# Kernel tuning notes

Hardware: AMD Instinct MI355X
Metric: run time of the kernel (lower is better)

## Reference

```python
import jax, jax.numpy as jnp
import numpy as np

B, H, W, C = 2, 128, 128, 192
HEADS = 6
HD = C // HEADS
WS = 16
OWIN = int(WS * 0.5) + WS          # 24
PAD = (OWIN - WS) // 2             # 4
NQ = WS * WS
NK = OWIN * OWIN
EPS = 1e-6
HID = ((int(C * 2.667) + 7) // 8) * 8  # 512


def _rel_pos_index():
    cq = np.stack(np.meshgrid(np.arange(WS), np.arange(WS), indexing='ij')).reshape(2, -1)
    ck = np.stack(np.meshgrid(np.arange(OWIN), np.arange(OWIN), indexing='ij')).reshape(2, -1)
    rel = (ck[:, None, :] - cq[:, :, None]).transpose(1, 2, 0).astype(np.int64)  # (nq, nk, 2)
    rel[:, :, 0] += WS - 1
    rel[:, :, 1] += WS - 1
    rel[:, :, 0] *= WS + OWIN - 1
    return rel.sum(-1)  # (nq, nk)

RPI = jnp.asarray(_rel_pos_index())


def setup_inputs() -> dict:
    key = jax.random.key(0)
    ks = jax.random.split(key, 16)
    def w(k, shape, s=0.02):
        return jax.random.normal(k, shape, jnp.float32) * s
    return {
        'x': jax.random.normal(ks[0], (B, H * W, C), jnp.float32),
        'qkv_w': w(ks[1], (3 * C, C)), 'qkv_b': jnp.zeros((3 * C,), jnp.float32),
        'proj_w': w(ks[2], (C, C)), 'proj_b': jnp.zeros((C,), jnp.float32),
        'rpb': w(ks[3], ((WS + OWIN - 1) ** 2, HEADS)),
        'n1_w': jnp.ones((C,), jnp.float32), 'n1_b': jnp.zeros((C,), jnp.float32),
        'ls1': jnp.full((C,), 1e-6, jnp.float32),
        'n2_w': jnp.ones((C,), jnp.float32), 'n2_b': jnp.zeros((C,), jnp.float32),
        'ls2': jnp.full((C,), 1e-6, jnp.float32),
        'fcgv_w': w(ks[4], (2 * HID, C)), 'fcgv_b': jnp.zeros((2 * HID,), jnp.float32),
        'dw_w': w(ks[5], (HID, 1, 3, 3)), 'dw_b': jnp.zeros((HID,), jnp.float32),
        'dwd_w': w(ks[6], (HID, 1, 3, 3)), 'dwd_b': jnp.zeros((HID,), jnp.float32),
        'dil_scale': w(ks[7], (1,), 0.1),
        'fco_w': w(ks[8], (C, HID)), 'fco_b': jnp.zeros((C,), jnp.float32),
    }


def _iln(x, wgt, bias):
    # spatially-holistic LN: stats over (L, C); returns normed x and residual scale
    xf = x.astype(jnp.float32)
    mean = xf.mean(axis=(1, 2), keepdims=True)
    var = ((xf - mean) ** 2).mean(axis=(1, 2), keepdims=True)
    std = jnp.sqrt(var + EPS)
    scale = jnp.minimum(std, 2.0)  # std_ema buffer initialized to 1.0 (eval path)
    xn = (xf - mean) / scale
    return (xn * wgt + bias).astype(x.dtype), scale


def _oca(x, qkv_w, qkv_b, proj_w, proj_b, rpb):
    b = x.shape[0]
    nh, nw = H // WS, W // WS
    nwin = b * nh * nw
    qkv = x @ qkv_w.T + qkv_b
    q, k, v = jnp.split(qkv, 3, axis=-1)
    # non-overlapping query windows: (nwin, heads, nq, hd)
    qw = q.reshape(b, nh, WS, nw, WS, C).transpose(0, 1, 3, 2, 4, 5)
    qw = qw.reshape(nwin, NQ, HEADS, HD).transpose(0, 2, 1, 3)
    # overlapping K/V windows via unfold(kernel=OWIN, stride=WS, pad=PAD)
    kv = jnp.concatenate([k, v], axis=-1).reshape(b, H, W, 2 * C).transpose(0, 3, 1, 2)
    kvp = jnp.pad(kv, ((0, 0), (0, 0), (PAD, PAD), (PAD, PAD)))
    ih = (jnp.arange(nh) * WS)[:, None] + jnp.arange(OWIN)[None, :]
    iw = (jnp.arange(nw) * WS)[:, None] + jnp.arange(OWIN)[None, :]
    kvw = kvp[:, :, ih][:, :, :, :, iw]               # (b, 2C, nh, owin, nw, owin)
    kvw = kvw.transpose(0, 2, 4, 3, 5, 1).reshape(nwin, NK, 2 * C)
    kw = kvw[..., :C].reshape(nwin, NK, HEADS, HD).transpose(0, 2, 1, 3)
    vw = kvw[..., C:].reshape(nwin, NK, HEADS, HD).transpose(0, 2, 1, 3)
    bias = rpb[RPI].transpose(2, 0, 1)                # (heads, nq, nk)
    logits = jnp.einsum('whqd,whkd->whqk', qw, kw) * (HD ** -0.5) + bias
    attn = jax.nn.softmax(logits, axis=-1)
    out = jnp.einsum('whqk,whkd->whqd', attn, vw)
    out = out.transpose(0, 2, 1, 3).reshape(nwin, NQ, C) @ proj_w.T + proj_b
    # window reverse -> (b, H*W, C)
    out = out.reshape(b, nh, nw, WS, WS, C).transpose(0, 1, 3, 2, 4, 5).reshape(b, H * W, C)
    return out


def _dw(x, wgt, bias, dil):
    y = jax.lax.conv_general_dilated(x, wgt, (1, 1), [(dil, dil), (dil, dil)],
                                     rhs_dilation=(dil, dil), feature_group_count=HID)
    return y + bias[None, :, None, None]


def _ffn(x, fcgv_w, fcgv_b, dw_w, dw_b, dwd_w, dwd_b, dil_scale, fco_w, fco_b):
    gv = x @ fcgv_w.T + fcgv_b
    g, val = jnp.split(gv, 2, axis=-1)
    h = jax.nn.silu(g) * val
    h = h.transpose(0, 2, 1).reshape(-1, HID, H, W)
    h = _dw(h, dw_w, dw_b, 1)
    h = h + dil_scale[0] * _dw(h, dwd_w, dwd_b, 2)
    h = h.reshape(-1, HID, H * W).transpose(0, 2, 1)
    return h @ fco_w.T + fco_b


def reference(x, qkv_w, qkv_b, proj_w, proj_b, rpb, n1_w, n1_b, ls1, n2_w, n2_b, ls2,
              fcgv_w, fcgv_b, dw_w, dw_b, dwd_w, dwd_b, dil_scale, fco_w, fco_b):
    xn, std1 = _iln(x, n1_w, n1_b)
    x = x + std1 * (ls1 * _oca(xn, qkv_w, qkv_b, proj_w, proj_b, rpb))
    xn2, std2 = _iln(x, n2_w, n2_b)
    x = x + std2 * (ls2 * _ffn(xn2, fcgv_w, fcgv_b, dw_w, dw_b, dwd_w, dwd_b, dil_scale, fco_w, fco_b))
    return x
```

## Files before the change

### kernel.cpp

```cpp
#include <hip/hip_runtime.h>

#define DI __device__ __forceinline__

typedef __attribute__((ext_vector_type(8))) short bh8;
typedef __attribute__((ext_vector_type(4))) float fx4;
typedef __attribute__((ext_vector_type(16))) float fx16;

DI short f2bf(float f) {
  unsigned u = __builtin_bit_cast(unsigned, f);
  u += 0x7FFFu + ((u >> 16) & 1u);
  return (short)(u >> 16);
}
DI float bf2f(short s) {
  unsigned u = ((unsigned)(unsigned short)s) << 16;
  return __builtin_bit_cast(float, u);
}
DI fx4 mfma16(bh8 a, bh8 b, fx4 c) {
  return __builtin_amdgcn_mfma_f32_16x16x32_bf16(a, b, c, 0, 0, 0);
}
DI fx16 mfma32(bh8 a, bh8 b, fx16 c) {
  return __builtin_amdgcn_mfma_f32_32x32x16_bf16(a, b, c, 0, 0, 0);
}
DI fx4 fzero() { fx4 z = {0.f, 0.f, 0.f, 0.f}; return z; }

DI float fexp2(float x) {
#if __has_builtin(__builtin_amdgcn_exp2f)
  return __builtin_amdgcn_exp2f(x);
#else
  return exp2f(x);
#endif
}

DI bh8 pack8(const float* src) {
  fx4 v0 = *(const fx4*)src;
  fx4 v1 = *(const fx4*)(src + 4);
  bh8 pk;
#pragma unroll
  for (int j = 0; j < 4; j++) { pk[j] = f2bf(v0[j]); pk[j + 4] = f2bf(v1[j]); }
  return pk;
}
DI bh8 pack8_aff(const float* src, const float* affc) {
  fx4 v0 = *(const fx4*)src;
  fx4 v1 = *(const fx4*)(src + 4);
  bh8 pk;
#pragma unroll
  for (int j = 0; j < 4; j++) {
    pk[j]     = f2bf(v0[j] * affc[2 * j]       + affc[2 * j + 1]);
    pk[j + 4] = f2bf(v1[j] * affc[2 * (j + 4)] + affc[2 * (j + 4) + 1]);
  }
  return pk;
}

__global__ __launch_bounds__(256) void iln_partial(const float* __restrict__ x,
                                                   float* __restrict__ part) {
  const int blk = blockIdx.x, tid = threadIdx.x;
  const fx4* p = (const fx4*)(x + (size_t)blk * 12288);
  float s = 0.f, s2 = 0.f;
#pragma unroll
  for (int i = 0; i < 12; i++) {
    fx4 v = p[i * 256 + tid];
    s  += v[0] + v[1] + v[2] + v[3];
    s2 += v[0] * v[0] + v[1] * v[1] + v[2] * v[2] + v[3] * v[3];
  }
  __shared__ float sm[512];
  sm[tid] = s; sm[256 + tid] = s2;
  __syncthreads();
  for (int st = 128; st > 0; st >>= 1) {
    if (tid < st) { sm[tid] += sm[tid + st]; sm[256 + tid] += sm[256 + tid + st]; }
    __syncthreads();
  }
  if (tid == 0) { part[blk * 2] = sm[0]; part[blk * 2 + 1] = sm[256]; }
}

__global__ __launch_bounds__(256) void iln_final(const float* __restrict__ part,
                                                 const float* __restrict__ w,
                                                 const float* __restrict__ bias,
                                                 float* __restrict__ aff,
                                                 float* __restrict__ st) {
  const int b = blockIdx.x, tid = threadIdx.x;
  __shared__ float sm[512];
  sm[tid]       = part[(b * 256 + tid) * 2];
  sm[256 + tid] = part[(b * 256 + tid) * 2 + 1];
  __syncthreads();
  for (int s = 128; s > 0; s >>= 1) {
    if (tid < s) { sm[tid] += sm[tid + s]; sm[256 + tid] += sm[256 + tid + s]; }
    __syncthreads();
  }
  const float invn = 1.f / 3145728.f;
  float mean = sm[0] * invn;
  float var  = sm[256] * invn - mean * mean;
  float scale = fminf(sqrtf(var + 1e-6f), 2.f);
  if (tid < 192) {
    float a = w[tid] / scale;
    aff[(b * 192 + tid) * 2]     = a;
    aff[(b * 192 + tid) * 2 + 1] = bias[tid] - mean * a;
  }
  if (tid == 0) { st[b * 2] = mean; st[b * 2 + 1] = scale; }
}

__global__ __launch_bounds__(256) void cvt_w(const float* __restrict__ qkv_w,
                                             const float* __restrict__ proj_w,
                                             const float* __restrict__ fcgv_w,
                                             const float* __restrict__ fco_w,
                                             short* __restrict__ wbuf) {
  int t = blockIdx.x * 256 + threadIdx.x;
  int blk = t >> 6, lane = t & 63;
  int g = lane >> 4, h = lane & 15;
  const float* src;
  if (blk < 216) {
    int b2 = blk;
    int ni = b2 % 3; b2 /= 3;
    int wn = b2 & 1; b2 >>= 1;
    int kt = b2 % 6; b2 /= 6;
    int nt = b2;
    src = qkv_w + (size_t)(nt * 96 + wn * 48 + ni * 16 + h) * 192 + kt * 32 + g * 8;
  } else if (blk < 288) {
    int b2 = blk - 216;
    int ni = b2 % 3; b2 /= 3;
    int wn = b2 & 1; b2 >>= 1;
    int kt = b2 % 6; b2 /= 6;
    int nt = b2;
    src = proj_w + (size_t)(nt * 96 + wn * 48 + ni * 16 + h) * 192 + kt * 32 + g * 8;
  } else if (blk < 672) {
    int b2 = blk - 288;
    int gv = b2 & 1; b2 >>= 1;
    int ni = b2 & 1; b2 >>= 1;
    int wn = b2 & 1; b2 >>= 1;
    int kt = b2 % 6; b2 /= 6;
    int nt = b2;
    int r = wn * 32 + ni * 16 + h;
    int row = gv ? (512 + nt * 64 + r) : (nt * 64 + r);
    src = fcgv_w + (size_t)row * 192 + kt * 32 + g * 8;
  } else {
    int b2 = blk - 672;
    int ni = b2 % 3; b2 /= 3;
    int wn = b2 & 1; b2 >>= 1;
    int kt = b2 & 15; b2 >>= 4;
    int nt = b2;
    src = fco_w + (size_t)(nt * 96 + wn * 48 + ni * 16 + h) * 512 + kt * 32 + g * 8;
  }
  *(bh8*)(wbuf + (size_t)blk * 512 + lane * 8) = pack8(src);
}

__global__ __launch_bounds__(256) void cvt_aff(const float* __restrict__ src,
                                               const float* __restrict__ aff,
                                               short* __restrict__ dst) {
  int t = blockIdx.x * 256 + threadIdx.x;
  int row = t / 24;
  int c0 = (t - row * 24) * 8;
  const float* affp = aff + (row >> 14) * 384 + c0 * 2;
  int mt = row >> 7, wm = (row >> 6) & 1, mi = (row >> 4) & 3, h = row & 15;
  int kt = c0 >> 5, g = (c0 >> 3) & 3;
  int blk = ((mt * 2 + wm) * 4 + mi) * 6 + kt;
  int lane = g * 16 + h;
  *(bh8*)(dst + (size_t)blk * 512 + lane * 8) = pack8_aff(src + (size_t)row * 192 + c0, affp);
}

__global__ __launch_bounds__(256) void bias_gen(const float* __restrict__ rpb,
                                                float* __restrict__ btf) {
  int t = blockIdx.x * 256 + threadIdx.x;
  int lane = t & 63;
  int u = t >> 6;
  int qi = u & 1; int u2 = u >> 1;
  int ki = u2 & 1; u2 >>= 1;
  int kc = u2 % 9; u2 = u2 / 9;
  int w = u2 & 3, head = u2 >> 2;
  int c = lane & 31, hi = lane >> 5;
  int q = w * 64 + qi * 32 + c;
  int qterm = (q >> 4) * 39 + (q & 15);
  (void)ki; (void)kc;
  float o[16];
#pragma unroll
  for (int r = 0; r < 16; r++) {
    int kk = ((u >> 2) % 9) * 64 + ((u >> 1) & 1) * 32 + (r & 3) + 8 * (r >> 2) + 4 * hi;
    int ky = (kk * 2731) >> 16;
    int kx = kk - ky * 24;
    int idx = ky * 39 + kx + 600 - qterm;
    o[r] = rpb[idx * 6 + head] * 1.4426950408889634f;
  }
  fx4* dst = (fx4*)btf;
#pragma unroll
  for (int j = 0; j < 4; j++) {
    fx4 v = {o[4 * j], o[4 * j + 1], o[4 * j + 2], o[4 * j + 3]};
    dst[((size_t)u * 4 + j) * 64 + lane] = v;
  }
}

__global__ __launch_bounds__(256) void gemm_qkv(const short* __restrict__ xn,
                                                const short* __restrict__ wq,
                                                const float* __restrict__ wb,
                                                short* __restrict__ qb,
                                                short* __restrict__ kb,
                                                short* __restrict__ vb) {
  const int mt = blockIdx.x, by = blockIdx.y;
  const int m0 = mt * 128;
  const int tid = threadIdx.x, wid = tid >> 6, lane = tid & 63;
  const int g = lane >> 4, h = lane & 15;
  const int wm = wid >> 1, wn = wid & 1;
  fx4 acc[4][3];
#pragma unroll
  for (int i = 0; i < 4; i++)
#pragma unroll
    for (int j = 0; j < 3; j++) acc[i][j] = fzero();

#pragma unroll
  for (int kt = 0; kt < 6; kt++) {
    bh8 af[4], bf[3];
#pragma unroll
    for (int mi = 0; mi < 4; mi++)
      af[mi] = *(const bh8*)(xn + (size_t)((((mt * 2 + wm) * 4 + mi) * 6 + kt)) * 512 + lane * 8);
#pragma unroll
    for (int ni = 0; ni < 3; ni++)
      bf[ni] = *(const bh8*)(wq + (size_t)(((by * 6 + kt) * 2 + wn) * 3 + ni) * 512 + lane * 8);
#pragma unroll
    for (int ni = 0; ni < 3; ni++)
#pragma unroll
      for (int mi = 0; mi < 4; mi++) acc[mi][ni] = mfma16(af[mi], bf[ni], acc[mi][ni]);
  }
  const int seg = by >> 1;
  short* dst = (seg == 0) ? qb : (seg == 1 ? kb : vb);
  const float sc = (seg == 1) ? 0.25503486f : 1.0f;
  const int colbase = (by & 1) * 96;
#pragma unroll
  for (int mi = 0; mi < 4; mi++)
#pragma unroll
    for (int ni = 0; ni < 3; ni++)
#pragma unroll
      for (int r = 0; r < 4; r++) {
        int row = m0 + wm * 64 + mi * 16 + g * 4 + r;
        int col = colbase + wn * 48 + ni * 16 + h;
        dst[(size_t)row * 192 + col] = f2bf((acc[mi][ni][r] + wb[seg * 192 + col]) * sc);
      }
}

__global__ __launch_bounds__(256, 3) void attn_kernel(const short* __restrict__ qb,
                                                      const short* __restrict__ kb,
                                                      const short* __restrict__ vb,
                                                      const float* __restrict__ btf,
                                                      short* __restrict__ ao) {
  __shared__ short K_lds[64 * 40];
  __shared__ short Vt_lds[32 * 72];
  __shared__ float l_lds[256];
  const int tid = threadIdx.x;
  const int win = blockIdx.x, head = blockIdx.y;
  const int b = win >> 6, wy = (win >> 3) & 7, wx = win & 7;
  const int w = tid >> 6, lane = tid & 63, c = lane & 31, hi = lane >> 5;

  bh8 qf[2][2];
#pragma unroll
  for (int qi = 0; qi < 2; qi++) {
    int ql = w * 64 + qi * 32 + c;
    size_t gl = (size_t)(b * 16384 + (wy * 16 + (ql >> 4)) * 128 + wx * 16 + (ql & 15));
#pragma unroll
    for (int ds = 0; ds < 2; ds++)
      qf[qi][ds] = *(const bh8*)(qb + gl * 192 + head * 32 + ds * 16 + hi * 8);
  }
  float l_run[2] = {0.f, 0.f};
  fx16 out[2];
#pragma unroll
  for (int r = 0; r < 16; r++) { out[0][r] = 0.f; out[1][r] = 0.f; }

  const fx4* btf4 = (const fx4*)btf;
  const int hw9 = (head * 4 + w) * 9;

  const int kl_a = tid >> 2, part_a = tid & 3;
  const int kl_b = tid & 63, hg_b = tid >> 6;

  for (int kc = 0; kc < 9; kc++) {
    __syncthreads();
    {
      int key = kc * 64 + kl_a;
      int ky = key / 24, kx = key - ky * 24;
      int py = wy * 16 - 4 + ky, px = wx * 16 - 4 + kx;
      bh8 kv = {};
      if ((unsigned)py < 128u && (unsigned)px < 128u)
        kv = *(const bh8*)(kb + ((size_t)(b * 16384 + py * 128 + px)) * 192 + head * 32 + part_a * 8);
      *(bh8*)&K_lds[kl_a * 40 + part_a * 8] = kv;

      int key2 = kc * 64 + kl_b;
      int ky2 = key2 / 24, kx2 = key2 - ky2 * 24;
      int py2 = wy * 16 - 4 + ky2, px2 = wx * 16 - 4 + kx2;
      bh8 vv = {};
      if ((unsigned)py2 < 128u && (unsigned)px2 < 128u)
        vv = *(const bh8*)(vb + ((size_t)(b * 16384 + py2 * 128 + px2)) * 192 + head * 32 + hg_b * 8);
#pragma unroll
      for (int j = 0; j < 8; j++) Vt_lds[(hg_b * 8 + j) * 72 + kl_b] = vv[j];
    }
    __syncthreads();

    const fx4* base_kc = btf4 + (size_t)(hw9 + kc) * 1024 + lane;
#pragma unroll
    for (int ki = 0; ki < 2; ki++) {
      fx16 st[2];
#pragma unroll
      for (int qi = 0; qi < 2; qi++) {
        const fx4* bp = base_kc + (ki * 2 + qi) * 256;
        fx4 b0 = bp[0], b1 = bp[64], b2 = bp[128], b3 = bp[192];
#pragma unroll
        for (int m = 0; m < 4; m++) {
          st[qi][m]      = b0[m];
          st[qi][4 + m]  = b1[m];
          st[qi][8 + m]  = b2[m];
          st[qi][12 + m] = b3[m];
        }
      }
#pragma unroll
      for (int ds = 0; ds < 2; ds++) {
        bh8 kf = *(bh8*)&K_lds[(ki * 32 + c) * 40 + ds * 16 + hi * 8];
        st[0] = mfma32(kf, qf[0][ds], st[0]);
        st[1] = mfma32(kf, qf[1][ds], st[1]);
      }
#pragma unroll
      for (int qi = 0; qi < 2; qi++) {
        float s = 0.f;
#pragma unroll
        for (int r = 0; r < 16; r++) {
          float p = fexp2(st[qi][r]);
          st[qi][r] = p;
          s += p;
        }
        l_run[qi] += s;
      }
      int dwq[2][2][4];
#pragma unroll
      for (int qi = 0; qi < 2; qi++)
#pragma unroll
        for (int k1 = 0; k1 < 2; k1++)
#pragma unroll
          for (int p01 = 0; p01 < 2; p01++) {
            int rA = 2 * p01 + 8 * k1;
            int A, Bv;
            asm("v_cvt_pk_bf16_f32 %0, %1, %2" : "=v"(A)  : "v"(st[qi][rA]),     "v"(st[qi][rA + 1]));
            asm("v_cvt_pk_bf16_f32 %0, %1, %2" : "=v"(Bv) : "v"(st[qi][rA + 4]), "v"(st[qi][rA + 5]));
#if __has_builtin(__builtin_amdgcn_permlane32_swap)
            auto pr = __builtin_amdgcn_permlane32_swap((unsigned)A, (unsigned)Bv, false, false);
            dwq[qi][k1][p01]     = (int)pr[0];
            dwq[qi][k1][p01 + 2] = (int)pr[1];
#else
            int Ax = __shfl_xor(A, 32);
            int Bx = __shfl_xor(Bv, 32);
            dwq[qi][k1][p01]     = hi ? Bx : A;
            dwq[qi][k1][p01 + 2] = hi ? Bv : Ax;
#endif
          }
#pragma unroll
      for (int k1 = 0; k1 < 2; k1++) {
        bh8 bv2 = *(bh8*)&Vt_lds[c * 72 + (ki * 2 + k1) * 16 + hi * 8];
#pragma unroll
        for (int qi = 0; qi < 2; qi++) {
          int4 t4 = {dwq[qi][k1][0], dwq[qi][k1][1], dwq[qi][k1][2], dwq[qi][k1][3]};
          out[qi] = mfma32(__builtin_bit_cast(bh8, t4), bv2, out[qi]);
        }
      }
    }
  }
#pragma unroll
  for (int qi = 0; qi < 2; qi++) {
    float lp = l_run[qi] + __shfl_xor(l_run[qi], 32);
    l_lds[w * 64 + qi * 32 + c] = 1.f / lp;
  }
  __syncthreads();
#pragma unroll
  for (int qi = 0; qi < 2; qi++)
#pragma unroll
    for (int r = 0; r < 16; r++) {
      int row = (r & 3) + 8 * (r >> 2) + 4 * hi;
      float val = out[qi][r] * l_lds[w * 64 + qi * 32 + row];
      int ql = w * 64 + qi * 32 + row;
      ao[((size_t)(win * 256 + ql)) * 192 + head * 32 + c] = f2bf(val);
    }
}

__global__ __launch_bounds__(256) void gemm_proj(const short* __restrict__ ao,
                                                 const short* __restrict__ wp,
                                                 const float* __restrict__ wb,
                                                 const float* __restrict__ x,
                                                 const float* __restrict__ ls1,
                                                 const float* __restrict__ st,
                                                 float* __restrict__ x1,
                                                 float* __restrict__ part2) {
  __shared__ float red[512];
  const int m0 = blockIdx.x * 128, by = blockIdx.y;
  const int tid = threadIdx.x, wid = tid >> 6, lane = tid & 63;
  const int g = lane >> 4, h = lane & 15;
  const int wm = wid >> 1, wn = wid & 1;
  fx4 acc[4][3];
#pragma unroll
  for (int i = 0; i < 4; i++)
#pragma unroll
    for (int j = 0; j < 3; j++) acc[i][j] = fzero();

#pragma unroll
  for (int kt = 0; kt < 6; kt++) {
    bh8 af[4], bf[3];
#pragma unroll
    for (int mi = 0; mi < 4; mi++)
      af[mi] = *(const bh8*)(ao + (size_t)(m0 + wm * 64 + mi * 16 + h) * 192 + kt * 32 + g * 8);
#pragma unroll
    for (int ni = 0; ni < 3; ni++)
      bf[ni] = *(const bh8*)(wp + (size_t)(((by * 6 + kt) * 2 + wn) * 3 + ni) * 512 + lane * 8);
#pragma unroll
    for (int ni = 0; ni < 3; ni++)
#pragma unroll
      for (int mi = 0; mi < 4; mi++) acc[mi][ni] = mfma16(af[mi], bf[ni], acc[mi][ni]);
  }
  const int n0 = by * 96;
  float ps = 0.f, ps2 = 0.f;
#pragma unroll
  for (int mi = 0; mi < 4; mi++)
#pragma unroll
    for (int ni = 0; ni < 3; ni++)
#pragma unroll
      for (int r = 0; r < 4; r++) {
        int grow = m0 + wm * 64 + mi * 16 + g * 4 + r;
        int win = grow >> 8, q = grow & 255;
        int bb = win >> 6, wy = (win >> 3) & 7, wxx = win & 7;
        int l = (wy * 16 + (q >> 4)) * 128 + wxx * 16 + (q & 15);
        int col = n0 + wn * 48 + ni * 16 + h;
        size_t di = ((size_t)(bb * 16384 + l)) * 192 + col;
        float s1 = st[bb * 2 + 1];
        float val = x[di] + s1 * ls1[col] * (acc[mi][ni][r] + wb[col]);
        x1[di] = val;
        ps += val;
        ps2 += val * val;
      }
  red[tid] = ps; red[256 + tid] = ps2;
  __syncthreads();
  for (int s = 128; s > 0; s >>= 1) {
    if (tid < s) { red[tid] += red[tid + s]; red[256 + tid] += red[256 + tid + s]; }
    __syncthreads();
  }
  if (tid == 0) {
    int pi = blockIdx.x * 2 + by;
    part2[pi * 2] = red[0];
    part2[pi * 2 + 1] = red[256];
  }
}

__global__ __launch_bounds__(256) void gemm_fcgv(const short* __restrict__ x1n,
                                                 const short* __restrict__ wg,
                                                 const float* __restrict__ wb,
                                                 short* __restrict__ hp) {
  __shared__ short T[64 * 136];
  const int mt = blockIdx.x, by = blockIdx.y, n0 = by * 64;
  const int m0 = mt * 128;
  const int b = m0 >> 14, l0 = m0 & 16383;
  const int tid = threadIdx.x, wid = tid >> 6, lane = tid & 63;
  const int g = lane >> 4, h = lane & 15;
  const int wm = wid >> 1, wn = wid & 1;
  fx4 accg[4][2], accv[4][2];
#pragma unroll
  for (int i = 0; i < 4; i++)
#pragma unroll
    for (int j = 0; j < 2; j++) { accg[i][j] = fzero(); accv[i][j] = fzero(); }

#pragma unroll
  for (int kt = 0; kt < 6; kt++) {
    bh8 af[4], bg[2], bv[2];
#pragma unroll
    for (int mi = 0; mi < 4; mi++)
      af[mi] = *(const bh8*)(x1n + (size_t)((((mt * 2 + wm) * 4 + mi) * 6 + kt)) * 512 + lane * 8);
#pragma unroll
    for (int ni = 0; ni < 2; ni++) {
      size_t base = (size_t)((((by * 6 + kt) * 2 + wn) * 2 + ni) * 2) * 512;
      bg[ni] = *(const bh8*)(wg + base + lane * 8);
      bv[ni] = *(const bh8*)(wg + base + 512 + lane * 8);
    }
#pragma unroll
    for (int ni = 0; ni < 2; ni++)
#pragma unroll
      for (int mi = 0; mi < 4; mi++) {
        accg[mi][ni] = mfma16(af[mi], bg[ni], accg[mi][ni]);
        accv[mi][ni] = mfma16(af[mi], bv[ni], accv[mi][ni]);
      }
  }
  short hs[4][2][4];
#pragma unroll
  for (int mi = 0; mi < 4; mi++)
#pragma unroll
    for (int ni = 0; ni < 2; ni++)
#pragma unroll
      for (int r = 0; r < 4; r++) {
        int colg = n0 + wn * 32 + ni * 16 + h;
        float gv = accg[mi][ni][r] + wb[colg];
        float vv = accv[mi][ni][r] + wb[512 + colg];
        hs[mi][ni][r] = f2bf(gv / (1.f + __expf(-gv)) * vv);
      }
#pragma unroll
  for (int mi = 0; mi < 4; mi++)
#pragma unroll
    for (int ni = 0; ni < 2; ni++)
#pragma unroll
      for (int r = 0; r < 4; r++) {
        int cc = wn * 32 + ni * 16 + h;
        int rl = wm * 64 + mi * 16 + g * 4 + r;
        T[cc * 136 + rl] = hs[mi][ni][r];
      }
  __syncthreads();
#pragma unroll
  for (int i = 0; i < 4; i++) {
    int ch = tid + i * 256;
    int cc = ch >> 4, lg = ch & 15;
    bh8 v = *(bh8*)&T[cc * 136 + lg * 8];
    *(bh8*)(hp + (((size_t)(b * 512 + n0 + cc)) << 14) + l0 + lg * 8) = v;
  }
}

__global__ __launch_bounds__(256, 2) void dw_fused(const short* __restrict__ in,
                                                   const float* __restrict__ w1,
                                                   const float* __restrict__ b1,
                                                   const float* __restrict__ w2,
                                                   const float* __restrict__ b2,
                                                   const float* __restrict__ dsc,
                                                   short* __restrict__ outp) {
  __shared__ short P[136 * 128];
  __shared__ short D[136 * 128];
  const int p = blockIdx.x, c = p & 511;
  const int tid = threadIdx.x;
#pragma unroll
  for (int i = 0; i < 8; i++) {
    int gs = i * 256 + tid;
    int yy = gs >> 4, sl = gs & 15;
    bh8 v = *(const bh8*)(in + ((size_t)p << 14) + gs * 8);
    *(bh8*)&P[yy * 136 + sl * 8] = v;
  }
  float k1[9], k2[9];
#pragma unroll
  for (int j = 0; j < 9; j++) { k1[j] = w1[c * 9 + j]; k2[j] = w2[c * 9 + j]; }
  const float bias1 = b1[c], bias2 = b2[c], ds = dsc[0];
  const int y = tid >> 1, hf = tid & 1;
  __syncthreads();

#pragma unroll
  for (int g = 0; g < 8; g++) {
    const int x0 = hf * 64 + g * 8;
    float acc[8];
#pragma unroll
    for (int i = 0; i < 8; i++) acc[i] = bias1;
#pragma unroll
    for (int ky = 0; ky < 3; ky++) {
      int yy = y + ky - 1;
      if ((unsigned)yy < 128u) {
        const short* row = &P[yy * 136];
        float f[10];
        bh8 v = *(const bh8*)&row[x0];
#pragma unroll
        for (int j = 0; j < 8; j++) f[j + 1] = bf2f(v[j]);
        f[0] = (x0 == 0) ? 0.f : bf2f(row[x0 - 1]);
        f[9] = (x0 == 120) ? 0.f : bf2f(row[x0 + 8]);
        float w0 = k1[ky * 3], wA = k1[ky * 3 + 1], wB = k1[ky * 3 + 2];
#pragma unroll
        for (int i = 0; i < 8; i++) acc[i] += f[i] * w0 + f[i + 1] * wA + f[i + 2] * wB;
      }
    }
    bh8 pk;
#pragma unroll
    for (int i = 0; i < 8; i++) pk[i] = f2bf(acc[i]);
    *(bh8*)&D[y * 136 + x0] = pk;
  }
  __syncthreads();

#pragma unroll
  for (int g = 0; g < 8; g++) {
    const int x0 = hf * 64 + g * 8;
    float acc[8], center[8];
#pragma unroll
    for (int i = 0; i < 8; i++) acc[i] = bias2;
#pragma unroll
    for (int ky = 0; ky < 3; ky++) {
      int yy = y + (ky - 1) * 2;
      if ((unsigned)yy < 128u) {
        const short* row = &D[yy * 136];
        float f[12];
        bh8 v = *(const bh8*)&row[x0];
#pragma unroll
        for (int j = 0; j < 8; j++) f[j + 2] = bf2f(v[j]);
        if (x0 == 0) { f[0] = 0.f; f[1] = 0.f; }
        else {
          unsigned lp = *(const unsigned*)&row[x0 - 2];
          f[0] = __builtin_bit_cast(float, lp << 16);
          f[1] = __builtin_bit_cast(float, lp & 0xffff0000u);
        }
        if (x0 == 120) { f[10] = 0.f; f[11] = 0.f; }
        else {
          unsigned rp = *(const unsigned*)&row[x0 + 8];
          f[10] = __builtin_bit_cast(float, rp << 16);
          f[11] = __builtin_bit_cast(float, rp & 0xffff0000u);
        }
        float w0 = k2[ky * 3], wA = k2[ky * 3 + 1], wB = k2[ky * 3 + 2];
#pragma unroll
        for (int i = 0; i < 8; i++) acc[i] += f[i] * w0 + f[i + 2] * wA + f[i + 4] * wB;
        if (ky == 1) {
#pragma unroll
          for (int i = 0; i < 8; i++) center[i] = f[i + 2];
        }
      }
    }
    bh8 pk;
#pragma unroll
    for (int i = 0; i < 8; i++) pk[i] = f2bf(center[i] + ds * acc[i]);
    *(bh8*)(outp + ((size_t)p << 14) + y * 128 + x0) = pk;
  }
}

__global__ __launch_bounds__(256) void gemm_fco(const short* __restrict__ h2,
                                                const short* __restrict__ wo,
                                                const float* __restrict__ wb,
                                                const float* __restrict__ x1,
                                                const float* __restrict__ ls2,
                                                const float* __restrict__ st,
                                                float* __restrict__ out) {
  __shared__ short As[128 * 40];
  const int m0 = blockIdx.x * 128, by = blockIdx.y, n0 = by * 96;
  const int b = m0 >> 14, l0 = m0 & 16383;
  const int tid = threadIdx.x, wid = tid >> 6, lane = tid & 63;
  const int g = lane >> 4, h = lane & 15;
  const int wm = wid >> 1, wn = wid & 1;
  const int cp = tid & 15, lg = tid >> 4;
  fx4 acc[4][3];
#pragma unroll
  for (int i = 0; i < 4; i++)
#pragma unroll
    for (int j = 0; j < 3; j++) acc[i][j] = fzero();

  for (int kt = 0; kt < 16; kt++) {
    const int k0 = kt * 32;
    {
      const short* basep = h2 + (((size_t)(b * 512 + k0 + 2 * cp)) << 14) + l0 + lg * 8;
      bh8 v0 = *(const bh8*)basep;
      bh8 v1 = *(const bh8*)(basep + 16384);
#pragma unroll
      for (int j = 0; j < 8; j++) {
        unsigned pkv = (unsigned)(unsigned short)v0[j] | (((unsigned)(unsigned short)v1[j]) << 16);
        *(unsigned*)&As[(lg * 8 + j) * 40 + 2 * cp] = pkv;
      }
    }
    __syncthreads();
    bh8 af[4], bf[3];
#pragma unroll
    for (int mi = 0; mi < 4; mi++)
      af[mi] = *(bh8*)&As[(wm * 64 + mi * 16 + h) * 40 + g * 8];
#pragma unroll
    for (int ni = 0; ni < 3; ni++)
      bf[ni] = *(const bh8*)(wo + (size_t)(((by * 16 + kt) * 2 + wn) * 3 + ni) * 512 + lane * 8);
#pragma unroll
    for (int ni = 0; ni < 3; ni++)
#pragma unroll
      for (int mi = 0; mi < 4; mi++) acc[mi][ni] = mfma16(af[mi], bf[ni], acc[mi][ni]);
    __syncthreads();
  }
  float s2 = st[b * 2 + 1];
#pragma unroll
  for (int mi = 0; mi < 4; mi++)
#pragma unroll
    for (int ni = 0; ni < 3; ni++)
#pragma unroll
      for (int r = 0; r < 4; r++) {
        int row = m0 + wm * 64 + mi * 16 + g * 4 + r;
        int col = n0 + wn * 48 + ni * 16 + h;
        size_t di = (size_t)row * 192 + col;
        out[di] = x1[di] + s2 * ls2[col] * (acc[mi][ni][r] + wb[col]);
      }
}

extern "C" void kernel_launch(void* const* d_in, const int* in_sizes, int n_in,
                              void* d_out, int out_size, void* d_ws, size_t ws_size,
                              hipStream_t stream) {
  const float* x      = (const float*)d_in[0];
  const float* qkv_w  = (const float*)d_in[1];
  const float* qkv_b  = (const float*)d_in[2];
  const float* proj_w = (const float*)d_in[3];
  const float* proj_b = (const float*)d_in[4];
  const float* rpb    = (const float*)d_in[5];
  const float* n1_w   = (const float*)d_in[6];
  const float* n1_b   = (const float*)d_in[7];
  const float* ls1    = (const float*)d_in[8];
  const float* n2_w   = (const float*)d_in[9];
  const float* n2_b   = (const float*)d_in[10];
  const float* ls2    = (const float*)d_in[11];
  const float* fcgv_w = (const float*)d_in[12];
  const float* fcgv_b = (const float*)d_in[13];
  const float* dw_w   = (const float*)d_in[14];
  const float* dw_b   = (const float*)d_in[15];
  const float* dwd_w  = (const float*)d_in[16];
  const float* dwd_b  = (const float*)d_in[17];
  const float* dil    = (const float*)d_in[18];
  const float* fco_w  = (const float*)d_in[19];
  const float* fco_b  = (const float*)d_in[20];
  float* out = (float*)d_out;
  char* ws = (char*)d_ws;

  short* wbuf = (short*)(ws + 0);
  short* wq = wbuf;
  short* wp = wbuf + 110592;
  short* wg = wbuf + 147456;
  short* wo = wbuf + 344064;
  float* part  = (float*)(ws + 884736);
  float* aff1  = (float*)(ws + 888832);
  float* aff2  = (float*)(ws + 890368);
  float* st1   = (float*)(ws + 891904);
  float* st2   = (float*)(ws + 891968);
  float* part2 = (float*)(ws + 892032);
  short* xn  = (short*)(ws + 1048576);
  float* btf = (float*)(ws + 13631488);
  short* qb  = (short*)(ws + 17301504);
  short* kb  = (short*)(ws + 29884416);
  short* vb  = (short*)(ws + 42467328);
  short* ao  = (short*)(ws + 55050240);
  float* x1  = (float*)(ws + 1048576);
  short* x1n = (short*)(ws + 26214400);
  short* hp  = (short*)(ws + 42467328);

  cvt_w<<<216, 256, 0, stream>>>(qkv_w, proj_w, fcgv_w, fco_w, wbuf);
  iln_partial<<<512, 256, 0, stream>>>(x, part);
  iln_final<<<2, 256, 0, stream>>>(part, n1_w, n1_b, aff1, st1);
  cvt_aff<<<3072, 256, 0, stream>>>(x, aff1, xn);
  bias_gen<<<216, 256, 0, stream>>>(rpb, btf);
  gemm_qkv<<<dim3(256, 6), 256, 0, stream>>>(xn, wq, qkv_b, qb, kb, vb);
  attn_kernel<<<dim3(128, 6), 256, 0, stream>>>(qb, kb, vb, btf, ao);
  gemm_proj<<<dim3(256, 2), 256, 0, stream>>>(ao, wp, proj_b, x, ls1, st1, x1, part2);
  iln_final<<<2, 256, 0, stream>>>(part2, n2_w, n2_b, aff2, st2);
  cvt_aff<<<3072, 256, 0, stream>>>(x1, aff2, x1n);
  gemm_fcgv<<<dim3(256, 8), 256, 0, stream>>>(x1n, wg, fcgv_b, hp);
  dw_fused<<<1024, 256, 0, stream>>>(hp, dw_w, dw_b, dwd_w, dwd_b, dil, hp);
  gemm_fco<<<dim3(256, 2), 256, 0, stream>>>(hp, wo, fco_b, x1, ls2, st2, out);
}
```

Measured before the change: 185.2 us.

## Merge prep kernels, widen attention blocks, retile proj/fco GEMMs with double buffering

Merges the weight-conversion and bias-generation kernels into a single launch. Attention now runs 512-thread blocks where each wave owns 32 queries, and K and V loads are split across thread halves. The proj GEMM uses 64-row tiles so twice as many blocks launch, and iln_final takes a variable partial count to match. The fco GEMM uses 48-column tiles with a double-buffered LDS A-tile that prefetches the next k-slice. Together these aim to raise parallelism and latency hiding, at the cost of re-reading the weight fragments and more redundant A traffic.

```diff
diff --git a/kernel.cpp b/kernel.cpp
--- a/kernel.cpp
+++ b/kernel.cpp
@@ -73,14 +73,20 @@
 }
 
 __global__ __launch_bounds__(256) void iln_final(const float* __restrict__ part,
+                                                 int nper,
                                                  const float* __restrict__ w,
                                                  const float* __restrict__ bias,
                                                  float* __restrict__ aff,
                                                  float* __restrict__ st) {
   const int b = blockIdx.x, tid = threadIdx.x;
   __shared__ float sm[512];
-  sm[tid]       = part[(b * 256 + tid) * 2];
-  sm[256 + tid] = part[(b * 256 + tid) * 2 + 1];
+  float s0 = part[(b * nper + tid) * 2];
+  float s1 = part[(b * nper + tid) * 2 + 1];
+  if (nper == 512) {
+    s0 += part[(b * nper + 256 + tid) * 2];
+    s1 += part[(b * nper + 256 + tid) * 2 + 1];
+  }
+  sm[tid] = s0; sm[256 + tid] = s1;
   __syncthreads();
   for (int s = 128; s > 0; s >>= 1) {
     if (tid < s) { sm[tid] += sm[tid + s]; sm[256 + tid] += sm[256 + tid + s]; }
@@ -98,48 +104,77 @@
   if (tid == 0) { st[b * 2] = mean; st[b * 2 + 1] = scale; }
 }
 
-__global__ __launch_bounds__(256) void cvt_w(const float* __restrict__ qkv_w,
-                                             const float* __restrict__ proj_w,
-                                             const float* __restrict__ fcgv_w,
-                                             const float* __restrict__ fco_w,
-                                             short* __restrict__ wbuf) {
-  int t = blockIdx.x * 256 + threadIdx.x;
-  int blk = t >> 6, lane = t & 63;
-  int g = lane >> 4, h = lane & 15;
-  const float* src;
-  if (blk < 216) {
-    int b2 = blk;
-    int ni = b2 % 3; b2 /= 3;
-    int wn = b2 & 1; b2 >>= 1;
-    int kt = b2 % 6; b2 /= 6;
-    int nt = b2;
-    src = qkv_w + (size_t)(nt * 96 + wn * 48 + ni * 16 + h) * 192 + kt * 32 + g * 8;
-  } else if (blk < 288) {
-    int b2 = blk - 216;
-    int ni = b2 % 3; b2 /= 3;
-    int wn = b2 & 1; b2 >>= 1;
-    int kt = b2 % 6; b2 /= 6;
-    int nt = b2;
-    src = proj_w + (size_t)(nt * 96 + wn * 48 + ni * 16 + h) * 192 + kt * 32 + g * 8;
-  } else if (blk < 672) {
-    int b2 = blk - 288;
-    int gv = b2 & 1; b2 >>= 1;
-    int ni = b2 & 1; b2 >>= 1;
-    int wn = b2 & 1; b2 >>= 1;
-    int kt = b2 % 6; b2 /= 6;
-    int nt = b2;
-    int r = wn * 32 + ni * 16 + h;
-    int row = gv ? (512 + nt * 64 + r) : (nt * 64 + r);
-    src = fcgv_w + (size_t)row * 192 + kt * 32 + g * 8;
+__global__ __launch_bounds__(256) void prep_wb(const float* __restrict__ qkv_w,
+                                               const float* __restrict__ proj_w,
+                                               const float* __restrict__ fcgv_w,
+                                               const float* __restrict__ fco_w,
+                                               const float* __restrict__ rpb,
+                                               short* __restrict__ wbuf,
+                                               float* __restrict__ btf) {
+  if (blockIdx.x < 216) {
+    int t = blockIdx.x * 256 + threadIdx.x;
+    int blk = t >> 6, lane = t & 63;
+    int g = lane >> 4, h = lane & 15;
+    const float* src;
+    if (blk < 216) {
+      int b2 = blk;
+      int ni = b2 % 3; b2 /= 3;
+      int wn = b2 & 1; b2 >>= 1;
+      int kt = b2 % 6; b2 /= 6;
+      int nt = b2;
+      src = qkv_w + (size_t)(nt * 96 + wn * 48 + ni * 16 + h) * 192 + kt * 32 + g * 8;
+    } else if (blk < 288) {
+      int b2 = blk - 216;
+      int ni = b2 % 3; b2 /= 3;
+      int wn = b2 & 1; b2 >>= 1;
+      int kt = b2 % 6; b2 /= 6;
+      int nt = b2;
+      src = proj_w + (size_t)(nt * 96 + wn * 48 + ni * 16 + h) * 192 + kt * 32 + g * 8;
+    } else if (blk < 672) {
+      int b2 = blk - 288;
+      int gv = b2 & 1; b2 >>= 1;
+      int ni = b2 & 1; b2 >>= 1;
+      int wn = b2 & 1; b2 >>= 1;
+      int kt = b2 % 6; b2 /= 6;
+      int nt = b2;
+      int r = wn * 32 + ni * 16 + h;
+      int row = gv ? (512 + nt * 64 + r) : (nt * 64 + r);
+      src = fcgv_w + (size_t)row * 192 + kt * 32 + g * 8;
+    } else {
+      int b2 = blk - 672;
+      int ni = b2 % 3; b2 /= 3;
+      int wn = b2 & 1; b2 >>= 1;
+      int kt = b2 & 15; b2 >>= 4;
+      int nt = b2;
+      src = fco_w + (size_t)(nt * 96 + wn * 48 + ni * 16 + h) * 512 + kt * 32 + g * 8;
+    }
+    *(bh8*)(wbuf + (size_t)blk * 512 + lane * 8) = pack8(src);
   } else {
-    int b2 = blk - 672;
-    int ni = b2 % 3; b2 /= 3;
-    int wn = b2 & 1; b2 >>= 1;
-    int kt = b2 & 15; b2 >>= 4;
-    int nt = b2;
-    src = fco_w + (size_t)(nt * 96 + wn * 48 + ni * 16 + h) * 512 + kt * 32 + g * 8;
-  }
-  *(bh8*)(wbuf + (size_t)blk * 512 + lane * 8) = pack8(src);
+    int t = (blockIdx.x - 216) * 256 + threadIdx.x;
+    int lane = t & 63;
+    int u = t >> 6;
+    int hi = lane >> 5, c = lane & 31;
+    int qi = u & 1;
+    int w = (u >> 2) / 9 % 4;
+    int head = (u >> 2) / 36;
+    int q = w * 64 + qi * 32 + c;
+    int qterm = (q >> 4) * 39 + (q & 15);
+    float o[16];
+#pragma unroll
+    for (int r = 0; r < 16; r++) {
+      int kk = ((u >> 2) % 9) * 64 + ((u >> 1) & 1) * 32 + (r & 3) + 8 * (r >> 2) + 4 * hi;
+      int ky = (kk * 2731) >> 16;
+      int kx = kk - ky * 24;
+      int idx = ky * 39 + kx + 600 - qterm;
+      o[r] = rpb[idx * 6 + head] * 1.4426950408889634f;
+    }
+    fx4* dst = (fx4*)btf;
+#pragma unroll
+    for (int j = 0; j < 4; j++) {
+      fx4 v = {o[4 * j], o[4 * j + 1], o[4 * j + 2], o[4 * j + 3]};
+      dst[((size_t)u * 4 + j) * 64 + lane] = v;
+    }
+  }
 }
 
 __global__ __launch_bounds__(256) void cvt_aff(const float* __restrict__ src,
@@ -156,36 +191,6 @@
   *(bh8*)(dst + (size_t)blk * 512 + lane * 8) = pack8_aff(src + (size_t)row * 192 + c0, affp);
 }
 
-__global__ __launch_bounds__(256) void bias_gen(const float* __restrict__ rpb,
-                                                float* __restrict__ btf) {
-  int t = blockIdx.x * 256 + threadIdx.x;
-  int lane = t & 63;
-  int u = t >> 6;
-  int qi = u & 1; int u2 = u >> 1;
-  int ki = u2 & 1; u2 >>= 1;
-  int kc = u2 % 9; u2 = u2 / 9;
-  int w = u2 & 3, head = u2 >> 2;
-  int c = lane & 31, hi = lane >> 5;
-  int q = w * 64 + qi * 32 + c;
-  int qterm = (q >> 4) * 39 + (q & 15);
-  (void)ki; (void)kc;
-  float o[16];
-#pragma unroll
-  for (int r = 0; r < 16; r++) {
-    int kk = ((u >> 2) % 9) * 64 + ((u >> 1) & 1) * 32 + (r & 3) + 8 * (r >> 2) + 4 * hi;
-    int ky = (kk * 2731) >> 16;
-    int kx = kk - ky * 24;
-    int idx = ky * 39 + kx + 600 - qterm;
-    o[r] = rpb[idx * 6 + head] * 1.4426950408889634f;
-  }
-  fx4* dst = (fx4*)btf;
-#pragma unroll
-  for (int j = 0; j < 4; j++) {
-    fx4 v = {o[4 * j], o[4 * j + 1], o[4 * j + 2], o[4 * j + 3]};
-    dst[((size_t)u * 4 + j) * 64 + lane] = v;
-  }
-}
-
 __global__ __launch_bounds__(256) void gemm_qkv(const short* __restrict__ xn,
                                                 const short* __restrict__ wq,
                                                 const float* __restrict__ wb,
@@ -233,7 +238,7 @@
       }
 }
 
-__global__ __launch_bounds__(256, 3) void attn_kernel(const short* __restrict__ qb,
+__global__ __launch_bounds__(512, 4) void attn_kernel(const short* __restrict__ qb,
                                                       const short* __restrict__ kb,
                                                       const short* __restrict__ vb,
                                                       const float* __restrict__ btf,
@@ -245,30 +250,31 @@
   const int win = blockIdx.x, head = blockIdx.y;
   const int b = win >> 6, wy = (win >> 3) & 7, wx = win & 7;
   const int w = tid >> 6, lane = tid & 63, c = lane & 31, hi = lane >> 5;
-
-  bh8 qf[2][2];
-#pragma unroll
-  for (int qi = 0; qi < 2; qi++) {
-    int ql = w * 64 + qi * 32 + c;
+  const int qi = w & 1;
+
+  bh8 qf[2];
+  {
+    int ql = w * 32 + c;
     size_t gl = (size_t)(b * 16384 + (wy * 16 + (ql >> 4)) * 128 + wx * 16 + (ql & 15));
 #pragma unroll
     for (int ds = 0; ds < 2; ds++)
-      qf[qi][ds] = *(const bh8*)(qb + gl * 192 + head * 32 + ds * 16 + hi * 8);
-  }
-  float l_run[2] = {0.f, 0.f};
-  fx16 out[2];
-#pragma unroll
-  for (int r = 0; r < 16; r++) { out[0][r] = 0.f; out[1][r] = 0.f; }
+      qf[ds] = *(const bh8*)(qb + gl * 192 + head * 32 + ds * 16 + hi * 8);
+  }
+  float l_run = 0.f;
+  fx16 out;
+#pragma unroll
+  for (int r = 0; r < 16; r++) out[r] = 0.f;
 
   const fx4* btf4 = (const fx4*)btf;
-  const int hw9 = (head * 4 + w) * 9;
-
-  const int kl_a = tid >> 2, part_a = tid & 3;
-  const int kl_b = tid & 63, hg_b = tid >> 6;
+  const int hw9 = (head * 4 + (w >> 1)) * 9;
+
+  const bool isK = tid < 256;
+  const int kl_a = (tid & 255) >> 2, part_a = tid & 3;
+  const int kl_b = tid & 63, hg_b = (tid >> 6) & 3;
 
   for (int kc = 0; kc < 9; kc++) {
     __syncthreads();
-    {
+    if (isK) {
       int key = kc * 64 + kl_a;
       int ky = key / 24, kx = key - ky * 24;
       int py = wy * 16 - 4 + ky, px = wx * 16 - 4 + kx;
@@ -276,7 +282,7 @@
       if ((unsigned)py < 128u && (unsigned)px < 128u)
         kv = *(const bh8*)(kb + ((size_t)(b * 16384 + py * 128 + px)) * 192 + head * 32 + part_a * 8);
       *(bh8*)&K_lds[kl_a * 40 + part_a * 8] = kv;
-
+    } else {
       int key2 = kc * 64 + kl_b;
       int ky2 = key2 / 24, kx2 = key2 - ky2 * 24;
       int py2 = wy * 16 - 4 + ky2, px2 = wx * 16 - 4 + kx2;
@@ -288,87 +294,80 @@
     }
     __syncthreads();
 
-    const fx4* base_kc = btf4 + (size_t)(hw9 + kc) * 1024 + lane;
+    const fx4* base_kc = btf4 + (size_t)(hw9 + kc) * 1024 + qi * 256 + lane;
 #pragma unroll
     for (int ki = 0; ki < 2; ki++) {
-      fx16 st[2];
-#pragma unroll
-      for (int qi = 0; qi < 2; qi++) {
-        const fx4* bp = base_kc + (ki * 2 + qi) * 256;
+      fx16 st;
+      {
+        const fx4* bp = base_kc + ki * 512;
         fx4 b0 = bp[0], b1 = bp[64], b2 = bp[128], b3 = bp[192];
 #pragma unroll
         for (int m = 0; m < 4; m++) {
-          st[qi][m]      = b0[m];
-          st[qi][4 + m]  = b1[m];
-          st[qi][8 + m]  = b2[m];
-          st[qi][12 + m] = b3[m];
+          st[m]      = b0[m];
+          st[4 + m]  = b1[m];
+          st[8 + m]  = b2[m];
+          st[12 + m] = b3[m];
         }
       }
 #pragma unroll
       for (int ds = 0; ds < 2; ds++) {
         bh8 kf = *(bh8*)&K_lds[(ki * 32 + c) * 40 + ds * 16 + hi * 8];
-        st[0] = mfma32(kf, qf[0][ds], st[0]);
-        st[1] = mfma32(kf, qf[1][ds], st[1]);
-      }
-#pragma unroll
-      for (int qi = 0; qi < 2; qi++) {
-        float s = 0.f;
+        st = mfma32(kf, qf[ds], st);
+      }
+      {
+        float s[16];
 #pragma unroll
         for (int r = 0; r < 16; r++) {
-          float p = fexp2(st[qi][r]);
-          st[qi][r] = p;
-          s += p;
+          float p = fexp2(st[r]);
+          st[r] = p;
+          s[r] = p;
         }
-        l_run[qi] += s;
-      }
-      int dwq[2][2][4];
-#pragma unroll
-      for (int qi = 0; qi < 2; qi++)
-#pragma unroll
-        for (int k1 = 0; k1 < 2; k1++)
-#pragma unroll
-          for (int p01 = 0; p01 < 2; p01++) {
-            int rA = 2 * p01 + 8 * k1;
-            int A, Bv;
-            asm("v_cvt_pk_bf16_f32 %0, %1, %2" : "=v"(A)  : "v"(st[qi][rA]),     "v"(st[qi][rA + 1]));
-            asm("v_cvt_pk_bf16_f32 %0, %1, %2" : "=v"(Bv) : "v"(st[qi][rA + 4]), "v"(st[qi][rA + 5]));
+#pragma unroll
+        for (int d = 1; d < 16; d <<= 1)
+#pragma unroll
+          for (int r = 0; r < 16; r += 2 * d) s[r] += s[r + d];
+        l_run += s[0];
+      }
+      int dwq[2][4];
+#pragma unroll
+      for (int k1 = 0; k1 < 2; k1++)
+#pragma unroll
+        for (int p01 = 0; p01 < 2; p01++) {
+          int rA = 2 * p01 + 8 * k1;
+          int A, Bv;
+          asm("v_cvt_pk_bf16_f32 %0, %1, %2" : "=v"(A)  : "v"(st[rA]),     "v"(st[rA + 1]));
+          asm("v_cvt_pk_bf16_f32 %0, %1, %2" : "=v"(Bv) : "v"(st[rA + 4]), "v"(st[rA + 5]));
 #if __has_builtin(__builtin_amdgcn_permlane32_swap)
-            auto pr = __builtin_amdgcn_permlane32_swap((unsigned)A, (unsigned)Bv, false, false);
-            dwq[qi][k1][p01]     = (int)pr[0];
-            dwq[qi][k1][p01 + 2] = (int)pr[1];
+          auto pr = __builtin_amdgcn_permlane32_swap((unsigned)A, (unsigned)Bv, false, false);
+          dwq[k1][p01]     = (int)pr[0];
+          dwq[k1][p01 + 2] = (int)pr[1];
 #else
-            int Ax = __shfl_xor(A, 32);
-            int Bx = __shfl_xor(Bv, 32);
-            dwq[qi][k1][p01]     = hi ? Bx : A;
-            dwq[qi][k1][p01 + 2] = hi ? Bv : Ax;
+          int Ax = __shfl_xor(A, 32);
+          int Bx = __shfl_xor(Bv, 32);
+          dwq[k1][p01]     = hi ? Bx : A;
+          dwq[k1][p01 + 2] = hi ? Bv : Ax;
 #endif
-          }
+        }
 #pragma unroll
       for (int k1 = 0; k1 < 2; k1++) {
         bh8 bv2 = *(bh8*)&Vt_lds[c * 72 + (ki * 2 + k1) * 16 + hi * 8];
-#pragma unroll
-        for (int qi = 0; qi < 2; qi++) {
-          int4 t4 = {dwq[qi][k1][0], dwq[qi][k1][1], dwq[qi][k1][2], dwq[qi][k1][3]};
-          out[qi] = mfma32(__builtin_bit_cast(bh8, t4), bv2, out[qi]);
-        }
-      }
-    }
-  }
-#pragma unroll
-  for (int qi = 0; qi < 2; qi++) {
-    float lp = l_run[qi] + __shfl_xor(l_run[qi], 32);
-    l_lds[w * 64 + qi * 32 + c] = 1.f / lp;
+        int4 t4 = {dwq[k1][0], dwq[k1][1], dwq[k1][2], dwq[k1][3]};
+        out = mfma32(__builtin_bit_cast(bh8, t4), bv2, out);
+      }
+    }
+  }
+  {
+    float lp = l_run + __shfl_xor(l_run, 32);
+    l_lds[w * 32 + c] = 1.f / lp;
   }
   __syncthreads();
 #pragma unroll
-  for (int qi = 0; qi < 2; qi++)
-#pragma unroll
-    for (int r = 0; r < 16; r++) {
-      int row = (r & 3) + 8 * (r >> 2) + 4 * hi;
-      float val = out[qi][r] * l_lds[w * 64 + qi * 32 + row];
-      int ql = w * 64 + qi * 32 + row;
-      ao[((size_t)(win * 256 + ql)) * 192 + head * 32 + c] = f2bf(val);
-    }
+  for (int r = 0; r < 16; r++) {
+    int row = (r & 3) + 8 * (r >> 2) + 4 * hi;
+    float val = out[r] * l_lds[w * 32 + row];
+    int ql = w * 32 + row;
+    ao[((size_t)(win * 256 + ql)) * 192 + head * 32 + c] = f2bf(val);
+  }
 }
 
 __global__ __launch_bounds__(256) void gemm_proj(const short* __restrict__ ao,
@@ -380,39 +379,39 @@
                                                  float* __restrict__ x1,
                                                  float* __restrict__ part2) {
   __shared__ float red[512];
-  const int m0 = blockIdx.x * 128, by = blockIdx.y;
+  const int m0 = blockIdx.x * 64, by = blockIdx.y;
   const int tid = threadIdx.x, wid = tid >> 6, lane = tid & 63;
   const int g = lane >> 4, h = lane & 15;
   const int wm = wid >> 1, wn = wid & 1;
-  fx4 acc[4][3];
-#pragma unroll
-  for (int i = 0; i < 4; i++)
+  fx4 acc[2][3];
+#pragma unroll
+  for (int i = 0; i < 2; i++)
 #pragma unroll
     for (int j = 0; j < 3; j++) acc[i][j] = fzero();
 
 #pragma unroll
   for (int kt = 0; kt < 6; kt++) {
-    bh8 af[4], bf[3];
-#pragma unroll
-    for (int mi = 0; mi < 4; mi++)
-      af[mi] = *(const bh8*)(ao + (size_t)(m0 + wm * 64 + mi * 16 + h) * 192 + kt * 32 + g * 8);
+    bh8 af[2], bf[3];
+#pragma unroll
+    for (int mi = 0; mi < 2; mi++)
+      af[mi] = *(const bh8*)(ao + (size_t)(m0 + wm * 32 + mi * 16 + h) * 192 + kt * 32 + g * 8);
 #pragma unroll
     for (int ni = 0; ni < 3; ni++)
       bf[ni] = *(const bh8*)(wp + (size_t)(((by * 6 + kt) * 2 + wn) * 3 + ni) * 512 + lane * 8);
 #pragma unroll
     for (int ni = 0; ni < 3; ni++)
 #pragma unroll
-      for (int mi = 0; mi < 4; mi++) acc[mi][ni] = mfma16(af[mi], bf[ni], acc[mi][ni]);
+      for (int mi = 0; mi < 2; mi++) acc[mi][ni] = mfma16(af[mi], bf[ni], acc[mi][ni]);
   }
   const int n0 = by * 96;
   float ps = 0.f, ps2 = 0.f;
 #pragma unroll
-  for (int mi = 0; mi < 4; mi++)
+  for (int mi = 0; mi < 2; mi++)
 #pragma unroll
     for (int ni = 0; ni < 3; ni++)
 #pragma unroll
       for (int r = 0; r < 4; r++) {
-        int grow = m0 + wm * 64 + mi * 16 + g * 4 + r;
+        int grow = m0 + wm * 32 + mi * 16 + g * 4 + r;
         int win = grow >> 8, q = grow & 255;
         int bb = win >> 6, wy = (win >> 3) & 7, wxx = win & 7;
         int l = (wy * 16 + (q >> 4)) * 128 + wxx * 16 + (q & 15);
@@ -610,54 +609,64 @@
                                                 const float* __restrict__ ls2,
                                                 const float* __restrict__ st,
                                                 float* __restrict__ out) {
-  __shared__ short As[128 * 40];
-  const int m0 = blockIdx.x * 128, by = blockIdx.y, n0 = by * 96;
+  __shared__ short As[2][128 * 40];
+  const int m0 = blockIdx.x * 128, by = blockIdx.y;
   const int b = m0 >> 14, l0 = m0 & 16383;
   const int tid = threadIdx.x, wid = tid >> 6, lane = tid & 63;
   const int g = lane >> 4, h = lane & 15;
-  const int wm = wid >> 1, wn = wid & 1;
+  const int wm = wid;
   const int cp = tid & 15, lg = tid >> 4;
-  fx4 acc[4][3];
-#pragma unroll
-  for (int i = 0; i < 4; i++)
+  fx4 acc[2][3];
+#pragma unroll
+  for (int i = 0; i < 2; i++)
 #pragma unroll
     for (int j = 0; j < 3; j++) acc[i][j] = fzero();
 
+  auto loadA = [&](int kt, bh8& v0, bh8& v1) {
+    const short* basep = h2 + (((size_t)(b * 512 + kt * 32 + 2 * cp)) << 14) + l0 + lg * 8;
+    v0 = *(const bh8*)basep;
+    v1 = *(const bh8*)(basep + 16384);
+  };
+  auto writeA = [&](int buf, bh8 v0, bh8 v1) {
+#pragma unroll
+    for (int j = 0; j < 8; j++) {
+      unsigned pkv = (unsigned)(unsigned short)v0[j] | (((unsigned)(unsigned short)v1[j]) << 16);
+      *(unsigned*)&As[buf][(lg * 8 + j) * 40 + 2 * cp] = pkv;
+    }
+  };
+  {
+    bh8 c0, c1;
+    loadA(0, c0, c1);
+    writeA(0, c0, c1);
+  }
+  int cur = 0;
   for (int kt = 0; kt < 16; kt++) {
-    const int k0 = kt * 32;
-    {
-      const short* basep = h2 + (((size_t)(b * 512 + k0 + 2 * cp)) << 14) + l0 + lg * 8;
-      bh8 v0 = *(const bh8*)basep;
-      bh8 v1 = *(const bh8*)(basep + 16384);
-#pragma unroll
-      for (int j = 0; j < 8; j++) {
-        unsigned pkv = (unsigned)(unsigned short)v0[j] | (((unsigned)(unsigned short)v1[j]) << 16);
-        *(unsigned*)&As[(lg * 8 + j) * 40 + 2 * cp] = pkv;
-      }
-    }
     __syncthreads();
-    bh8 af[4], bf[3];
-#pragma unroll
-    for (int mi = 0; mi < 4; mi++)
-      af[mi] = *(bh8*)&As[(wm * 64 + mi * 16 + h) * 40 + g * 8];
-#pragma unroll
-    for (int ni = 0; ni < 3; ni++)
-      bf[ni] = *(const bh8*)(wo + (size_t)(((by * 16 + kt) * 2 + wn) * 3 + ni) * 512 + lane * 8);
-#pragma unroll
-    for (int ni = 0; ni < 3; ni++)
-#pragma unroll
-      for (int mi = 0; mi < 4; mi++) acc[mi][ni] = mfma16(af[mi], bf[ni], acc[mi][ni]);
-    __syncthreads();
+    bh8 n0v, n1v;
+    if (kt < 15) loadA(kt + 1, n0v, n1v);
+    bh8 af[2], bf[3];
+#pragma unroll
+    for (int mi = 0; mi < 2; mi++)
+      af[mi] = *(bh8*)&As[cur][(wm * 32 + mi * 16 + h) * 40 + g * 8];
+#pragma unroll
+    for (int ni = 0; ni < 3; ni++)
+      bf[ni] = *(const bh8*)(wo + (size_t)((((by >> 1) * 16 + kt) * 2 + (by & 1)) * 3 + ni) * 512 + lane * 8);
+#pragma unroll
+    for (int ni = 0; ni < 3; ni++)
+#pragma unroll
+      for (int mi = 0; mi < 2; mi++) acc[mi][ni] = mfma16(af[mi], bf[ni], acc[mi][ni]);
+    if (kt < 15) writeA(cur ^ 1, n0v, n1v);
+    cur ^= 1;
   }
   float s2 = st[b * 2 + 1];
 #pragma unroll
-  for (int mi = 0; mi < 4; mi++)
+  for (int mi = 0; mi < 2; mi++)
 #pragma unroll
     for (int ni = 0; ni < 3; ni++)
 #pragma unroll
       for (int r = 0; r < 4; r++) {
-        int row = m0 + wm * 64 + mi * 16 + g * 4 + r;
-        int col = n0 + wn * 48 + ni * 16 + h;
+        int row = m0 + wm * 32 + mi * 16 + g * 4 + r;
+        int col = by * 48 + ni * 16 + h;
         size_t di = (size_t)row * 192 + col;
         out[di] = x1[di] + s2 * ls2[col] * (acc[mi][ni][r] + wb[col]);
       }
@@ -711,17 +720,16 @@
   short* x1n = (short*)(ws + 26214400);
   short* hp  = (short*)(ws + 42467328);
 
-  cvt_w<<<216, 256, 0, stream>>>(qkv_w, proj_w, fcgv_w, fco_w, wbuf);
+  prep_wb<<<432, 256, 0, stream>>>(qkv_w, proj_w, fcgv_w, fco_w, rpb, wbuf, btf);
   iln_partial<<<512, 256, 0, stream>>>(x, part);
-  iln_final<<<2, 256, 0, stream>>>(part, n1_w, n1_b, aff1, st1);
+  iln_final<<<2, 256, 0, stream>>>(part, 256, n1_w, n1_b, aff1, st1);
   cvt_aff<<<3072, 256, 0, stream>>>(x, aff1, xn);
-  bias_gen<<<216, 256, 0, stream>>>(rpb, btf);
   gemm_qkv<<<dim3(256, 6), 256, 0, stream>>>(xn, wq, qkv_b, qb, kb, vb);
-  attn_kernel<<<dim3(128, 6), 256, 0, stream>>>(qb, kb, vb, btf, ao);
-  gemm_proj<<<dim3(256, 2), 256, 0, stream>>>(ao, wp, proj_b, x, ls1, st1, x1, part2);
-  iln_final<<<2, 256, 0, stream>>>(part2, n2_w, n2_b, aff2, st2);
+  attn_kernel<<<dim3(128, 6), 512, 0, stream>>>(qb, kb, vb, btf, ao);
+  gemm_proj<<<dim3(512, 2), 256, 0, stream>>>(ao, wp, proj_b, x, ls1, st1, x1, part2);
+  iln_final<<<2, 256, 0, stream>>>(part2, 512, n2_w, n2_b, aff2, st2);
   cvt_aff<<<3072, 256, 0, stream>>>(x1, aff2, x1n);
   gemm_fcgv<<<dim3(256, 8), 256, 0, stream>>>(x1n, wg, fcgv_b, hp);
   dw_fused<<<1024, 256, 0, stream>>>(hp, dw_w, dw_b, dwd_w, dwd_b, dil, hp);
-  gemm_fco<<<dim3(256, 2), 256, 0, stream>>>(hp, wo, fco_b, x1, ls2, st2, out);
-}
+  gemm_fco<<<dim3(256, 4), 256, 0, stream>>>(hp, wo, fco_b, x1, ls2, st2, out);
+}
```

Result: slower. 196.9 us (+6.3%).
